# Kernel tuning notes

Hardware: AMD Instinct MI355X
Metric: run time of the kernel (lower is better)

The kernel has to match this reference:

```python
import jax, jax.numpy as jnp
import numpy as np

B, N, DIM, H, DH, EDGE_DIM = 2, 320, 512, 8, 64, 64
INNER = H * DH  # 512


def setup_inputs() -> dict:
    key = jax.random.key(0)
    ks = jax.random.split(key, 8)
    s = jnp.float32(0.02)
    f32 = jnp.float32
    return {
        "nodes": jax.random.normal(ks[0], (B, N, DIM), f32),
        "edges": jax.random.normal(ks[1], (B, EDGE_DIM, N, N), f32),
        "W_exp": jax.random.normal(ks[2], (DIM, INNER), f32) * s,
        "b_exp": jnp.zeros((INNER,), f32),
        "W_q": jax.random.normal(ks[3], (INNER, INNER), f32) * s,
        "b_q": jnp.zeros((INNER,), f32),
        "W_kv": jax.random.normal(ks[4], (INNER, 2 * INNER), f32) * s,
        "b_kv": jnp.zeros((2 * INNER,), f32),
        "W_e": jax.random.normal(ks[5], (EDGE_DIM, INNER), f32) * s,
        "b_e": jnp.zeros((INNER,), f32),
        "W_out": jax.random.normal(ks[6], (INNER, DIM), f32) * s,
        "b_out": jnp.zeros((DIM,), f32),
    }


def reference(nodes, edges, W_exp, b_exp, W_q, b_q, W_kv, b_kv, W_e, b_e, W_out, b_out):
    b, n, _ = nodes.shape
    h, dh = H, DH
    scale = dh ** -0.5

    x = nodes @ W_exp + b_exp                      # [b, n, inner]
    q = x @ W_q + b_q                              # [b, n, inner]
    kv = x @ W_kv + b_kv
    k, v = jnp.split(kv, 2, axis=-1)               # each [b, n, inner]

    def split_heads(t):
        return t.reshape(b, n, h, dh).transpose(0, 2, 1, 3)  # [b, h, n, dh]

    q, k, v = map(split_heads, (q, k, v))

    # edges: [b, edge_dim, i, j] -> projected edge k/v bias [b, h, i, j, dh]
    e = jnp.einsum('beij,ed->bijd', edges, W_e) + b_e
    e = e.reshape(b, n, n, h, dh).transpose(0, 3, 1, 2, 4)

    # sim = q . (k + e); split into matmul term + edge term (same math)
    sim = (jnp.einsum('bhid,bhjd->bhij', q, k)
           + jnp.einsum('bhid,bhijd->bhij', q, e)) * scale
    attn = jax.nn.softmax(sim, axis=-1)            # [b, h, i, j]

    # out = attn . (v + e)
    out = (jnp.einsum('bhij,bhjd->bhid', attn, v)
           + jnp.einsum('bhij,bhijd->bhid', attn, e))
    out = out.transpose(0, 2, 1, 3).reshape(b, n, h * dh)  # [b, n, inner]
    return out @ W_out + b_out
```

## Files before the change

kernel.cpp:

```cpp
#include <hip/hip_runtime.h>

#define B_  2
#define N_  320
#define H_  8
#define ED_ 64

typedef __attribute__((ext_vector_type(8))) short bf16x8;
typedef __attribute__((ext_vector_type(4))) float floatx4;

__device__ __forceinline__ ushort f2bf(float f) {
    union { float f; unsigned u; } c; c.f = f;
    unsigned u = c.u;
    return (ushort)((u + 0x7fffu + ((u >> 16) & 1u)) >> 16);
}
__device__ __forceinline__ float bf2f(ushort s) {
    union { unsigned u; float f; } c; c.u = ((unsigned)s) << 16;
    return c.f;
}
__device__ __forceinline__ uint4 packf8(const float* f) {
    uint4 r;
    r.x = (unsigned)f2bf(f[0]) | ((unsigned)f2bf(f[1]) << 16);
    r.y = (unsigned)f2bf(f[2]) | ((unsigned)f2bf(f[3]) << 16);
    r.z = (unsigned)f2bf(f[4]) | ((unsigned)f2bf(f[5]) << 16);
    r.w = (unsigned)f2bf(f[6]) | ((unsigned)f2bf(f[7]) << 16);
    return r;
}
__device__ __forceinline__ uint4 packu8(const ushort* s) {
    uint4 r;
    r.x = (unsigned)s[0] | ((unsigned)s[1] << 16);
    r.y = (unsigned)s[2] | ((unsigned)s[3] << 16);
    r.z = (unsigned)s[4] | ((unsigned)s[5] << 16);
    r.w = (unsigned)s[6] | ((unsigned)s[7] << 16);
    return r;
}

__global__ __launch_bounds__(256) void prep_kernel(
    const float* __restrict__ W_exp, const float* __restrict__ W_q,
    const float* __restrict__ W_kv, const float* __restrict__ W_out,
    const float* __restrict__ W_e,
    ushort* __restrict__ WT_exp, ushort* __restrict__ WT_qkv,
    ushort* __restrict__ WT_oh, ushort* __restrict__ WT_ol,
    float* __restrict__ W_eT, ushort* __restrict__ Wehi, ushort* __restrict__ Welo)
{
    __shared__ float T[64][65];
    const int id = blockIdx.x, tid = threadIdx.x;

    if (id >= 320) {
        const int c0 = (id - 320) * 64;
        const int r = tid >> 2, cs = (tid & 3) * 16;
        #pragma unroll
        for (int e = 0; e < 4; ++e) {
            float4 x4 = *(const float4*)&W_e[(long)r * 512 + c0 + cs + e * 4];
            T[r][cs + e*4] = x4.x; T[r][cs + e*4 + 1] = x4.y;
            T[r][cs + e*4 + 2] = x4.z; T[r][cs + e*4 + 3] = x4.w;
        }
        __syncthreads();
        const int cc = tid >> 2, ks = (tid & 3) * 16;
        const int hd = c0 + cc;
        float vals[16]; ushort hs[16], ls[16];
        #pragma unroll
        for (int e = 0; e < 16; ++e) {
            vals[e] = T[ks + e][cc];
            hs[e] = f2bf(vals[e]);
            ls[e] = f2bf(vals[e] - bf2f(hs[e]));
        }
        #pragma unroll
        for (int e = 0; e < 4; ++e) {
            float4 o4; o4.x = vals[e*4]; o4.y = vals[e*4+1]; o4.z = vals[e*4+2]; o4.w = vals[e*4+3];
            *(float4*)&W_eT[(long)hd * 64 + ks + e * 4] = o4;
        }
        *(uint4*)&Wehi[(long)hd * 64 + ks]     = packu8(hs);
        *(uint4*)&Wehi[(long)hd * 64 + ks + 8] = packu8(hs + 8);
        *(uint4*)&Welo[(long)hd * 64 + ks]     = packu8(ls);
        *(uint4*)&Welo[(long)hd * 64 + ks + 8] = packu8(ls + 8);
        return;
    }
    const float* src; ushort* dst; ushort* dstl = nullptr;
    int ldS, row0, kt, ct;
    if (id < 64)       { int l = id;       kt = l >> 3; ct = l & 7;  src = W_exp; ldS = 512;  dst = WT_exp; row0 = ct * 64; }
    else if (id < 128) { int l = id - 64;  kt = l >> 3; ct = l & 7;  src = W_q;   ldS = 512;  dst = WT_qkv; row0 = ct * 64; }
    else if (id < 256) { int l = id - 128; kt = l >> 4; ct = l & 15; src = W_kv;  ldS = 1024; dst = WT_qkv; row0 = 512 + ct * 64; }
    else               { int l = id - 256; kt = l >> 3; ct = l & 7;  src = W_out; ldS = 512;  dst = WT_oh; dstl = WT_ol; row0 = ct * 64; }
    const int k0 = kt * 64, c0 = ct * 64;
    {
        const int r = tid >> 2, cs = (tid & 3) * 16;
        #pragma unroll
        for (int e = 0; e < 4; ++e) {
            float4 x4 = *(const float4*)&src[(long)(k0 + r) * ldS + c0 + cs + e * 4];
            T[r][cs + e*4] = x4.x; T[r][cs + e*4 + 1] = x4.y;
            T[r][cs + e*4 + 2] = x4.z; T[r][cs + e*4 + 3] = x4.w;
        }
    }
    __syncthreads();
    {
        const int cc = tid >> 2, ks = (tid & 3) * 16;
        float vals[16];
        #pragma unroll
        for (int e = 0; e < 16; ++e) vals[e] = T[ks + e][cc];
        ushort* d = dst + (long)(row0 + cc) * 512 + k0 + ks;
        if (!dstl) {
            *(uint4*)d = packf8(vals);
            *(uint4*)(d + 8) = packf8(vals + 8);
        } else {
            ushort hs[16], ls[16];
            #pragma unroll
            for (int e = 0; e < 16; ++e) {
                hs[e] = f2bf(vals[e]);
                ls[e] = f2bf(vals[e] - bf2f(hs[e]));
            }
            *(uint4*)d = packu8(hs);
            *(uint4*)(d + 8) = packu8(hs + 8);
            ushort* d2 = dstl + (long)(row0 + cc) * 512 + k0 + ks;
            *(uint4*)d2 = packu8(ls);
            *(uint4*)(d2 + 8) = packu8(ls + 8);
        }
    }
}

template <int MODE>
__global__ __launch_bounds__(256) void gemm_v2(
    const void* __restrict__ Asrc, const ushort* __restrict__ WT,
    const float* __restrict__ bias1, const float* __restrict__ bias2,
    ushort* __restrict__ outbf, float* __restrict__ q_o,
    float* __restrict__ k_o, float* __restrict__ vt_o)
{
    __shared__ ushort As[64 * 64];
    __shared__ ushort Bs[64 * 64];
    __shared__ float  T[64][65];
    const int tid = threadIdx.x, lane = tid & 63, wid = tid >> 6;
    const int wr = wid >> 1, wc = wid & 1;
    const int bm = blockIdx.x * 64, bn = blockIdx.y * 64;
    const int srow = tid >> 2, sk = tid & 3;
    const int sw = (srow & 7) << 4;
    const int d1 = srow * 128 + ((sk * 32) ^ sw);
    const int d2 = srow * 128 + ((sk * 32 + 16) ^ sw);
    const ushort* Bsrc = WT + (long)(bn + srow) * 512 + sk * 16;

    floatx4 acc[2][2] = {};
    for (int k0 = 0; k0 < 512; k0 += 64) {
        uint4 a0, a1;
        if (MODE == 0) {
            const float* ap = (const float*)Asrc + (long)(bm + srow) * 512 + k0 + sk * 16;
            float f[16];
            #pragma unroll
            for (int e = 0; e < 4; ++e) {
                float4 x4 = *(const float4*)(ap + e * 4);
                f[e*4] = x4.x; f[e*4+1] = x4.y; f[e*4+2] = x4.z; f[e*4+3] = x4.w;
            }
            a0 = packf8(f); a1 = packf8(f + 8);
        } else {
            const ushort* ap = (const ushort*)Asrc + (long)(bm + srow) * 512 + k0 + sk * 16;
            a0 = *(const uint4*)ap; a1 = *(const uint4*)(ap + 8);
        }
        uint4 b0 = *(const uint4*)(Bsrc + k0);
        uint4 b1 = *(const uint4*)(Bsrc + k0 + 8);
        if (k0) __syncthreads();
        *(uint4*)((char*)As + d1) = a0;
        *(uint4*)((char*)As + d2) = a1;
        *(uint4*)((char*)Bs + d1) = b0;
        *(uint4*)((char*)Bs + d2) = b1;
        __syncthreads();
        #pragma unroll
        for (int s = 0; s < 2; ++s) {
            const int kb = s * 64 + ((lane >> 4) * 16);
            bf16x8 af[2], bfr[2];
            #pragma unroll
            for (int mf = 0; mf < 2; ++mf) {
                int row = wr * 32 + mf * 16 + (lane & 15);
                af[mf] = *(const bf16x8*)((const char*)As + row * 128 + (kb ^ ((row & 7) << 4)));
            }
            #pragma unroll
            for (int nf = 0; nf < 2; ++nf) {
                int col = wc * 32 + nf * 16 + (lane & 15);
                bfr[nf] = *(const bf16x8*)((const char*)Bs + col * 128 + (kb ^ ((col & 7) << 4)));
            }
            #pragma unroll
            for (int mf = 0; mf < 2; ++mf)
                #pragma unroll
                for (int nf = 0; nf < 2; ++nf)
                    acc[mf][nf] = __builtin_amdgcn_mfma_f32_16x16x32_bf16(
                        af[mf], bfr[nf], acc[mf][nf], 0, 0, 0);
        }
    }
    const int r4 = (lane >> 4) * 4, c16 = lane & 15;
    if (MODE == 0) {
        #pragma unroll
        for (int mf = 0; mf < 2; ++mf)
            #pragma unroll
            for (int nf = 0; nf < 2; ++nf)
                #pragma unroll
                for (int j = 0; j < 4; ++j) {
                    int row = bm + wr * 32 + mf * 16 + r4 + j;
                    int cn  = bn + wc * 32 + nf * 16 + c16;
                    outbf[(long)row * 512 + cn] = f2bf(acc[mf][nf][j] + bias1[cn]);
                }
    } else {
        const int cat = blockIdx.y >> 3;
        if (cat == 0) {
            #pragma unroll
            for (int mf = 0; mf < 2; ++mf)
                #pragma unroll
                for (int nf = 0; nf < 2; ++nf)
                    #pragma unroll
                    for (int j = 0; j < 4; ++j) {
                        int row = bm + wr * 32 + mf * 16 + r4 + j;
                        int cn  = bn + wc * 32 + nf * 16 + c16;
                        q_o[(long)row * 512 + cn] = acc[mf][nf][j] + bias1[cn];
                    }
        } else if (cat == 1) {
            #pragma unroll
            for (int mf = 0; mf < 2; ++mf)
                #pragma unroll
                for (int nf = 0; nf < 2; ++nf)
                    #pragma unroll
                    for (int j = 0; j < 4; ++j) {
                        int row = bm + wr * 32 + mf * 16 + r4 + j;
                        int cn  = bn + wc * 32 + nf * 16 + c16;
                        k_o[(long)row * 512 + (cn - 512)] = acc[mf][nf][j] + bias2[cn - 512];
                    }
        } else {
            #pragma unroll
            for (int mf = 0; mf < 2; ++mf)
                #pragma unroll
                for (int nf = 0; nf < 2; ++nf)
                    #pragma unroll
                    for (int j = 0; j < 4; ++j) {
                        int rl = wr * 32 + mf * 16 + r4 + j;
                        int cl = wc * 32 + nf * 16 + c16;
                        T[rl][cl] = acc[mf][nf][j] + bias2[bn - 512 + cl];
                    }
            __syncthreads();
            const int cl = tid >> 2, rl4 = (tid & 3) * 16;
            const int bb = bm / N_, ii0 = bm % N_, cv0 = bn - 1024;
            const long orow = (long)bb * 512 + cv0 + cl;
            #pragma unroll
            for (int e4 = 0; e4 < 4; ++e4) {
                float4 o4;
                o4.x = T[rl4 + e4*4 + 0][cl]; o4.y = T[rl4 + e4*4 + 1][cl];
                o4.z = T[rl4 + e4*4 + 2][cl]; o4.w = T[rl4 + e4*4 + 3][cl];
                *(float4*)&vt_o[orow * N_ + ii0 + rl4 + e4*4] = o4;
            }
        }
    }
}

__global__ __launch_bounds__(256) void k_qk(
    const float* __restrict__ q, const float* __restrict__ k,
    float* __restrict__ S_g)
{
    __shared__ ushort Qh[64 * 64], Ql[64 * 64], Kt[320 * 64];
    const int it = blockIdx.x, bh = blockIdx.y;
    const int b = bh >> 3, h = bh & 7;
    const int tid = threadIdx.x, lane = tid & 63, wid = tid >> 6;
    const int srow = tid >> 2, sk = tid & 3;
    const int sw = (srow & 7) << 4;
    const int d1 = srow * 128 + ((sk * 32) ^ sw);
    const int d2 = srow * 128 + ((sk * 32 + 16) ^ sw);

    {
        const float* ap = q + (long)(b * N_ + it * 64 + srow) * 512 + h * 64 + sk * 16;
        float f[16]; ushort hs[16], ls[16];
        #pragma unroll
        for (int e = 0; e < 4; ++e) {
            float4 x4 = *(const float4*)(ap + e * 4);
            f[e*4] = 0.125f * x4.x; f[e*4+1] = 0.125f * x4.y;
            f[e*4+2] = 0.125f * x4.z; f[e*4+3] = 0.125f * x4.w;
        }
        #pragma unroll
        for (int e = 0; e < 16; ++e) {
            hs[e] = f2bf(f[e]);
            ls[e] = f2bf(f[e] - bf2f(hs[e]));
        }
        *(uint4*)((char*)Qh + d1) = packu8(hs);
        *(uint4*)((char*)Qh + d2) = packu8(hs + 8);
        *(uint4*)((char*)Ql + d1) = packu8(ls);
        *(uint4*)((char*)Ql + d2) = packu8(ls + 8);
    }
    #pragma unroll
    for (int p = 0; p < 5; ++p) {
        const int row = p * 64 + srow;
        const float* kp = k + (long)(b * N_ + row) * 512 + h * 64 + sk * 16;
        float f[16];
        #pragma unroll
        for (int e = 0; e < 4; ++e) {
            float4 x4 = *(const float4*)(kp + e * 4);
            f[e*4] = x4.x; f[e*4+1] = x4.y; f[e*4+2] = x4.z; f[e*4+3] = x4.w;
        }
        *(uint4*)((char*)Kt + row * 128 + ((sk * 32) ^ sw))      = packf8(f);
        *(uint4*)((char*)Kt + row * 128 + ((sk * 32 + 16) ^ sw)) = packf8(f + 8);
    }
    __syncthreads();

    const int j0w = wid * 80;
    floatx4 acc[4][5] = {};
    #pragma unroll
    for (int s = 0; s < 2; ++s) {
        const int kb = s * 64 + ((lane >> 4) * 16);
        bf16x8 afh[4], afl[4], bf[5];
        #pragma unroll
        for (int mf = 0; mf < 4; ++mf) {
            int row = mf * 16 + (lane & 15);
            int off = row * 128 + (kb ^ ((row & 7) << 4));
            afh[mf] = *(const bf16x8*)((const char*)Qh + off);
            afl[mf] = *(const bf16x8*)((const char*)Ql + off);
        }
        #pragma unroll
        for (int jt = 0; jt < 5; ++jt) {
            int row = j0w + jt * 16 + (lane & 15);
            bf[jt] = *(const bf16x8*)((const char*)Kt + row * 128 + (kb ^ ((row & 7) << 4)));
        }
        #pragma unroll
        for (int mf = 0; mf < 4; ++mf)
            #pragma unroll
            for (int jt = 0; jt < 5; ++jt) {
                acc[mf][jt] = __builtin_amdgcn_mfma_f32_16x16x32_bf16(afh[mf], bf[jt], acc[mf][jt], 0, 0, 0);
                acc[mf][jt] = __builtin_amdgcn_mfma_f32_16x16x32_bf16(afl[mf], bf[jt], acc[mf][jt], 0, 0, 0);
            }
    }
    const int r4 = (lane >> 4) * 4, c16 = lane & 15;
    #pragma unroll
    for (int mf = 0; mf < 4; ++mf)
        #pragma unroll
        for (int jt = 0; jt < 5; ++jt)
            #pragma unroll
            for (int e = 0; e < 4; ++e) {
                int ri = it * 64 + mf * 16 + r4 + e;
                int cj = j0w + jt * 16 + c16;
                S_g[((long)bh * N_ + ri) * N_ + cj] = acc[mf][jt][e];
            }
}

__global__ __launch_bounds__(512) void attn_kernel(
    const float* __restrict__ q, const float* __restrict__ S_g,
    const float* __restrict__ edges, const float* __restrict__ W_eT,
    ushort* __restrict__ A_g, float* __restrict__ U_g)
{
    __shared__ ushort E_s[64 * 324];
    __shared__ ushort A_lds[8 * 320];
    __shared__ float  q_lds[512];
    __shared__ float  t_lds[512];

    const int blk = blockIdx.x;
    const int b = blk / N_, i = blk % N_;
    const int tid = threadIdx.x;
    const int w = tid >> 6, lane = tid & 63;

    q_lds[tid] = q[(long)blk * 512 + tid];
    {
        const float* ebase = edges + (long)b * ED_ * N_ * N_ + (long)i * N_;
        for (int idx = tid; idx < 64 * 80; idx += 512) {
            int c = idx / 80, j4 = (idx % 80) * 4;
            float4 e4 = *(const float4*)(ebase + (long)c * (N_ * N_) + j4);
            uint2 pk;
            pk.x = (unsigned)f2bf(e4.x) | ((unsigned)f2bf(e4.y) << 16);
            pk.y = (unsigned)f2bf(e4.z) | ((unsigned)f2bf(e4.w) << 16);
            *(uint2*)&E_s[c * 324 + j4] = pk;
        }
    }
    __syncthreads();

    {
        float tacc = 0.f;
        const float* we = W_eT + (long)(w * 64) * 64 + lane;
        const float* ql = q_lds + w * 64;
        #pragma unroll 8
        for (int d = 0; d < 64; ++d) tacc += ql[d] * we[(long)d * 64];
        t_lds[tid] = tacc;
    }
    __syncthreads();

    float sacc[5] = {0.f, 0.f, 0.f, 0.f, 0.f};
    {
        const float* tl = t_lds + w * 64;
        #pragma unroll 4
        for (int c = 0; c < 64; ++c) {
            float tc = tl[c];
            const ushort* er = &E_s[c * 324 + lane];
            sacc[0] += tc * bf2f(er[0]);
            sacc[1] += tc * bf2f(er[64]);
            sacc[2] += tc * bf2f(er[128]);
            sacc[3] += tc * bf2f(er[192]);
            sacc[4] += tc * bf2f(er[256]);
        }
    }
    const long sbase = ((long)(b * 8 + w) * N_ + i) * N_ + lane;
    const float scale = 0.125f;
    float s0 = sacc[0] * scale + S_g[sbase];
    float s1 = sacc[1] * scale + S_g[sbase + 64];
    float s2 = sacc[2] * scale + S_g[sbase + 128];
    float s3 = sacc[3] * scale + S_g[sbase + 192];
    float s4 = sacc[4] * scale + S_g[sbase + 256];

    float m = fmaxf(fmaxf(fmaxf(s0, s1), fmaxf(s2, s3)), s4);
    #pragma unroll
    for (int off = 32; off >= 1; off >>= 1) m = fmaxf(m, __shfl_xor(m, off, 64));
    s0 = __expf(s0 - m); s1 = __expf(s1 - m); s2 = __expf(s2 - m);
    s3 = __expf(s3 - m); s4 = __expf(s4 - m);
    float sum = s0 + s1 + s2 + s3 + s4;
    #pragma unroll
    for (int off = 32; off >= 1; off >>= 1) sum += __shfl_xor(sum, off, 64);
    float inv = 1.f / sum;
    ushort a0 = f2bf(s0 * inv), a1 = f2bf(s1 * inv), a2 = f2bf(s2 * inv),
           a3 = f2bf(s3 * inv), a4 = f2bf(s4 * inv);
    A_lds[w * 320 + lane]       = a0;
    A_lds[w * 320 + 64 + lane]  = a1;
    A_lds[w * 320 + 128 + lane] = a2;
    A_lds[w * 320 + 192 + lane] = a3;
    A_lds[w * 320 + 256 + lane] = a4;
    A_g[sbase]       = a0;
    A_g[sbase + 64]  = a1;
    A_g[sbase + 128] = a2;
    A_g[sbase + 192] = a3;
    A_g[sbase + 256] = a4;
    __syncthreads();

    float acc_u = 0.f;
    {
        const ushort* Er = E_s + lane * 324;
        const ushort* Ar = A_lds + w * 320;
        #pragma unroll 4
        for (int j4 = 0; j4 < 80; ++j4) {
            uint2 aa = *(const uint2*)&Ar[j4 * 4];
            uint2 e2 = *(const uint2*)&Er[j4 * 4];
            acc_u += bf2f((ushort)(aa.x & 0xffffu)) * bf2f((ushort)(e2.x & 0xffffu));
            acc_u += bf2f((ushort)(aa.x >> 16))     * bf2f((ushort)(e2.x >> 16));
            acc_u += bf2f((ushort)(aa.y & 0xffffu)) * bf2f((ushort)(e2.y & 0xffffu));
            acc_u += bf2f((ushort)(aa.y >> 16))     * bf2f((ushort)(e2.y >> 16));
        }
    }
    U_g[((long)(b * 8 + w) * N_ + i) * 64 + lane] = acc_u;
}

__global__ __launch_bounds__(256) void k_ov(
    const ushort* __restrict__ A_g, const float* __restrict__ vt,
    const float* __restrict__ U_g, const ushort* __restrict__ Wh_g,
    const ushort* __restrict__ Wl_g, const float* __restrict__ b_e,
    float* __restrict__ o_out)
{
    __shared__ ushort B0[64 * 64], B1[64 * 64], B2[64 * 64], B3[64 * 64];
    const int it = blockIdx.x, bh = blockIdx.y;
    const int b = bh >> 3, h = bh & 7;
    const int tid = threadIdx.x, lane = tid & 63, wid = tid >> 6;
    const int wr = wid >> 1, wc = wid & 1;
    const int srow = tid >> 2, sk = tid & 3;
    const int sw = (srow & 7) << 4;
    const int d1 = srow * 128 + ((sk * 32) ^ sw);
    const int d2 = srow * 128 + ((sk * 32 + 16) ^ sw);

    floatx4 acc[2][2] = {};
    for (int j0 = 0; j0 < 320; j0 += 64) {
        const ushort* ap = A_g + ((long)bh * N_ + it * 64 + srow) * N_ + j0 + sk * 16;
        uint4 a0 = *(const uint4*)ap, a1 = *(const uint4*)(ap + 8);
        const float* vp = vt + ((long)b * 512 + h * 64 + srow) * N_ + j0 + sk * 16;
        float f[16]; ushort hs[16], ls[16];
        #pragma unroll
        for (int e = 0; e < 4; ++e) {
            float4 x4 = *(const float4*)(vp + e * 4);
            f[e*4] = x4.x; f[e*4+1] = x4.y; f[e*4+2] = x4.z; f[e*4+3] = x4.w;
        }
        #pragma unroll
        for (int e = 0; e < 16; ++e) {
            hs[e] = f2bf(f[e]);
            ls[e] = f2bf(f[e] - bf2f(hs[e]));
        }
        if (j0) __syncthreads();
        *(uint4*)((char*)B0 + d1) = a0;
        *(uint4*)((char*)B0 + d2) = a1;
        *(uint4*)((char*)B1 + d1) = packu8(hs);
        *(uint4*)((char*)B1 + d2) = packu8(hs + 8);
        *(uint4*)((char*)B2 + d1) = packu8(ls);
        *(uint4*)((char*)B2 + d2) = packu8(ls + 8);
        __syncthreads();
        #pragma unroll
        for (int s = 0; s < 2; ++s) {
            const int kb = s * 64 + ((lane >> 4) * 16);
            bf16x8 af[2], bh_[2], bl_[2];
            #pragma unroll
            for (int mf = 0; mf < 2; ++mf) {
                int row = wr * 32 + mf * 16 + (lane & 15);
                af[mf] = *(const bf16x8*)((const char*)B0 + row * 128 + (kb ^ ((row & 7) << 4)));
            }
            #pragma unroll
            for (int nf = 0; nf < 2; ++nf) {
                int col = wc * 32 + nf * 16 + (lane & 15);
                int off = col * 128 + (kb ^ ((col & 7) << 4));
                bh_[nf] = *(const bf16x8*)((const char*)B1 + off);
                bl_[nf] = *(const bf16x8*)((const char*)B2 + off);
            }
            #pragma unroll
            for (int mf = 0; mf < 2; ++mf)
                #pragma unroll
                for (int nf = 0; nf < 2; ++nf) {
                    acc[mf][nf] = __builtin_amdgcn_mfma_f32_16x16x32_bf16(af[mf], bh_[nf], acc[mf][nf], 0, 0, 0);
                    acc[mf][nf] = __builtin_amdgcn_mfma_f32_16x16x32_bf16(af[mf], bl_[nf], acc[mf][nf], 0, 0, 0);
                }
        }
    }
    {
        const float* up = U_g + ((long)bh * N_ + it * 64 + srow) * 64 + sk * 16;
        float f[16]; ushort uh[16], ul[16];
        #pragma unroll
        for (int e = 0; e < 4; ++e) {
            float4 x4 = *(const float4*)(up + e * 4);
            f[e*4] = x4.x; f[e*4+1] = x4.y; f[e*4+2] = x4.z; f[e*4+3] = x4.w;
        }
        #pragma unroll
        for (int e = 0; e < 16; ++e) {
            uh[e] = f2bf(f[e]);
            ul[e] = f2bf(f[e] - bf2f(uh[e]));
        }
        const ushort* whp = Wh_g + ((long)h * 64 + srow) * 64 + sk * 16;
        const ushort* wlp = Wl_g + ((long)h * 64 + srow) * 64 + sk * 16;
        uint4 w0 = *(const uint4*)whp, w1 = *(const uint4*)(whp + 8);
        uint4 x0 = *(const uint4*)wlp, x1 = *(const uint4*)(wlp + 8);
        __syncthreads();
        *(uint4*)((char*)B0 + d1) = packu8(uh);
        *(uint4*)((char*)B0 + d2) = packu8(uh + 8);
        *(uint4*)((char*)B1 + d1) = packu8(ul);
        *(uint4*)((char*)B1 + d2) = packu8(ul + 8);
        *(uint4*)((char*)B2 + d1) = w0;
        *(uint4*)((char*)B2 + d2) = w1;
        *(uint4*)((char*)B3 + d1) = x0;
        *(uint4*)((char*)B3 + d2) = x1;
        __syncthreads();
        #pragma unroll
        for (int s = 0; s < 2; ++s) {
            const int kb = s * 64 + ((lane >> 4) * 16);
            bf16x8 ah[2], al[2], wh_[2], wl_[2];
            #pragma unroll
            for (int mf = 0; mf < 2; ++mf) {
                int row = wr * 32 + mf * 16 + (lane & 15);
                int off = row * 128 + (kb ^ ((row & 7) << 4));
                ah[mf] = *(const bf16x8*)((const char*)B0 + off);
                al[mf] = *(const bf16x8*)((const char*)B1 + off);
            }
            #pragma unroll
            for (int nf = 0; nf < 2; ++nf) {
                int col = wc * 32 + nf * 16 + (lane & 15);
                int off = col * 128 + (kb ^ ((col & 7) << 4));
                wh_[nf] = *(const bf16x8*)((const char*)B2 + off);
                wl_[nf] = *(const bf16x8*)((const char*)B3 + off);
            }
            #pragma unroll
            for (int mf = 0; mf < 2; ++mf)
                #pragma unroll
                for (int nf = 0; nf < 2; ++nf) {
                    acc[mf][nf] = __builtin_amdgcn_mfma_f32_16x16x32_bf16(ah[mf], wh_[nf], acc[mf][nf], 0, 0, 0);
                    acc[mf][nf] = __builtin_amdgcn_mfma_f32_16x16x32_bf16(al[mf], wh_[nf], acc[mf][nf], 0, 0, 0);
                    acc[mf][nf] = __builtin_amdgcn_mfma_f32_16x16x32_bf16(ah[mf], wl_[nf], acc[mf][nf], 0, 0, 0);
                }
        }
    }
    const int r4 = (lane >> 4) * 4, c16 = lane & 15;
    #pragma unroll
    for (int mf = 0; mf < 2; ++mf)
        #pragma unroll
        for (int nf = 0; nf < 2; ++nf)
            #pragma unroll
            for (int e = 0; e < 4; ++e) {
                int row = it * 64 + wr * 32 + mf * 16 + r4 + e;
                int col = wc * 32 + nf * 16 + c16;
                o_out[((long)(b * N_ + row)) * 512 + h * 64 + col] =
                    acc[mf][nf][e] + b_e[h * 64 + col];
            }
}

__global__ __launch_bounds__(256) void gemm_out(
    const float* __restrict__ Af, const ushort* __restrict__ BTh,
    const ushort* __restrict__ BTl, const float* __restrict__ bias,
    float* __restrict__ C)
{
    __shared__ ushort Ah[64 * 64], Al[64 * 64], Bh[64 * 64], Bl[64 * 64];
    const int tid = threadIdx.x, lane = tid & 63, wid = tid >> 6;
    const int wr = wid >> 1, wc = wid & 1;
    const int bm = blockIdx.x * 64, bn = blockIdx.y * 64;
    const int srow = tid >> 2, sk = tid & 3;
    const int sw = (srow & 7) << 4;
    const int d1 = srow * 128 + ((sk * 32) ^ sw);
    const int d2 = srow * 128 + ((sk * 32 + 16) ^ sw);
    const float*  asrc = Af + (long)(bm + srow) * 512 + sk * 16;
    const ushort* bhs  = BTh + (long)(bn + srow) * 512 + sk * 16;
    const ushort* bls  = BTl + (long)(bn + srow) * 512 + sk * 16;

    floatx4 acc[2][2] = {};
    for (int k0 = 0; k0 < 512; k0 += 64) {
        float f[16];
        #pragma unroll
        for (int e = 0; e < 4; ++e) {
            float4 x4 = *(const float4*)(asrc + k0 + e * 4);
            f[e*4] = x4.x; f[e*4+1] = x4.y; f[e*4+2] = x4.z; f[e*4+3] = x4.w;
        }
        ushort hs[16], ls[16];
        #pragma unroll
        for (int e = 0; e < 16; ++e) {
            hs[e] = f2bf(f[e]);
            ls[e] = f2bf(f[e] - bf2f(hs[e]));
        }
        uint4 bh0 = *(const uint4*)(bhs + k0);
        uint4 bh1 = *(const uint4*)(bhs + k0 + 8);
        uint4 bl0 = *(const uint4*)(bls + k0);
        uint4 bl1 = *(const uint4*)(bls + k0 + 8);
        if (k0) __syncthreads();
        *(uint4*)((char*)Ah + d1) = packu8(hs);
        *(uint4*)((char*)Ah + d2) = packu8(hs + 8);
        *(uint4*)((char*)Al + d1) = packu8(ls);
        *(uint4*)((char*)Al + d2) = packu8(ls + 8);
        *(uint4*)((char*)Bh + d1) = bh0;
        *(uint4*)((char*)Bh + d2) = bh1;
        *(uint4*)((char*)Bl + d1) = bl0;
        *(uint4*)((char*)Bl + d2) = bl1;
        __syncthreads();
        #pragma unroll
        for (int s = 0; s < 2; ++s) {
            const int kb = s * 64 + ((lane >> 4) * 16);
            bf16x8 ah[2], al[2], bh[2], bl[2];
            #pragma unroll
            for (int mf = 0; mf < 2; ++mf) {
                int row = wr * 32 + mf * 16 + (lane & 15);
                int off = row * 128 + (kb ^ ((row & 7) << 4));
                ah[mf] = *(const bf16x8*)((const char*)Ah + off);
                al[mf] = *(const bf16x8*)((const char*)Al + off);
            }
            #pragma unroll
            for (int nf = 0; nf < 2; ++nf) {
                int col = wc * 32 + nf * 16 + (lane & 15);
                int off = col * 128 + (kb ^ ((col & 7) << 4));
                bh[nf] = *(const bf16x8*)((const char*)Bh + off);
                bl[nf] = *(const bf16x8*)((const char*)Bl + off);
            }
            #pragma unroll
            for (int mf = 0; mf < 2; ++mf)
                #pragma unroll
                for (int nf = 0; nf < 2; ++nf) {
                    acc[mf][nf] = __builtin_amdgcn_mfma_f32_16x16x32_bf16(ah[mf], bh[nf], acc[mf][nf], 0, 0, 0);
                    acc[mf][nf] = __builtin_amdgcn_mfma_f32_16x16x32_bf16(ah[mf], bl[nf], acc[mf][nf], 0, 0, 0);
                    acc[mf][nf] = __builtin_amdgcn_mfma_f32_16x16x32_bf16(al[mf], bh[nf], acc[mf][nf], 0, 0, 0);
                }
        }
    }
    const int r4 = (lane >> 4) * 4, c16 = lane & 15;
    #pragma unroll
    for (int mf = 0; mf < 2; ++mf)
        #pragma unroll
        for (int nf = 0; nf < 2; ++nf)
            #pragma unroll
            for (int j = 0; j < 4; ++j) {
                int row = bm + wr * 32 + mf * 16 + r4 + j;
                int col = bn + wc * 32 + nf * 16 + c16;
                C[(long)row * 512 + col] = acc[mf][nf][j] + bias[col];
            }
}

extern "C" void kernel_launch(void* const* d_in, const int* in_sizes, int n_in,
                              void* d_out, int out_size, void* d_ws, size_t ws_size,
                              hipStream_t stream)
{
    const float* nodes = (const float*)d_in[0];
    const float* edges = (const float*)d_in[1];
    const float* W_exp = (const float*)d_in[2];
    const float* b_exp = (const float*)d_in[3];
    const float* W_q   = (const float*)d_in[4];
    const float* b_q   = (const float*)d_in[5];
    const float* W_kv  = (const float*)d_in[6];
    const float* b_kv  = (const float*)d_in[7];
    const float* W_e   = (const float*)d_in[8];
    const float* b_e   = (const float*)d_in[9];
    const float* W_out = (const float*)d_in[10];
    const float* b_out = (const float*)d_in[11];
    float* out = (float*)d_out;

    const long SZ = (long)B_ * N_ * 512;
    float* ws   = (float*)d_ws;
    float* q    = ws;
    float* k    = ws + SZ;
    float* v_t  = ws + 2 * SZ;
    float* U_g  = ws + 3 * SZ;
    float* S    = ws + 3 * SZ + 131072;
    float* o    = S;
    ushort* A_g    = (ushort*)(S + 1638400);
    ushort* x_bf   = A_g + 1638400;
    ushort* WT_exp = x_bf + SZ;
    ushort* WT_qkv = WT_exp + 262144;
    ushort* WT_oh  = WT_qkv + 786432;
    ushort* WT_ol  = WT_oh + 262144;
    float*  W_eT   = (float*)(WT_ol + 262144);
    ushort* Wehi   = (ushort*)(W_eT + 32768);
    ushort* Welo   = Wehi + 32768;

    prep_kernel<<<328, 256, 0, stream>>>(W_exp, W_q, W_kv, W_out, W_e,
                                         WT_exp, WT_qkv, WT_oh, WT_ol,
                                         W_eT, Wehi, Welo);
    gemm_v2<0><<<dim3(10, 8), 256, 0, stream>>>(nodes, WT_exp, b_exp, nullptr,
                                                x_bf, nullptr, nullptr, nullptr);
    gemm_v2<1><<<dim3(10, 24), 256, 0, stream>>>(x_bf, WT_qkv, b_q, b_kv,
                                                 nullptr, q, k, v_t);
    k_qk<<<dim3(5, 16), 256, 0, stream>>>(q, k, S);
    attn_kernel<<<640, 512, 0, stream>>>(q, S, edges, W_eT, A_g, U_g);
    k_ov<<<dim3(5, 16), 256, 0, stream>>>(A_g, v_t, U_g, Wehi, Welo, b_e, o);
    gemm_out<<<dim3(10, 8), 256, 0, stream>>>(o, WT_oh, WT_ol, b_out, out);
}
```

Before: 177.2 us.

## Store q/k/v as head-major bf16 and use MFMA for edge-score and edge-value terms

The QKV GEMM epilogue now writes q (pre-scaled by 1/sqrt(dh)), k and v directly as bf16 in head-major layout. This removes the fp32 round trips and the hi/lo split-bf16 conversions in k_qk and k_ov, which also halves their MFMA count. In attn_kernel, the edge-score dot product (t·E) and the A·E edge-value reduction move from scalar FMA loops to bf16 MFMA tiles, with partial scores staged in LDS. The cost is lower precision, since q, v and t now go through a single bf16 instead of the hi+lo pair, and attn_kernel uses more LDS.

New measurement: 162.6 us. -8.2%, faster.

```diff
diff --git a/kernel.cpp b/kernel.cpp
--- a/kernel.cpp
+++ b/kernel.cpp
@@ -32,6 +32,9 @@
     r.z = (unsigned)s[4] | ((unsigned)s[5] << 16);
     r.w = (unsigned)s[6] | ((unsigned)s[7] << 16);
     return r;
+}
+__device__ __forceinline__ bf16x8 u4bf(uint4 u) {
+    union { uint4 u; bf16x8 b; } c; c.u = u; return c.b;
 }
 
 __global__ __launch_bounds__(256) void prep_kernel(
@@ -121,8 +124,8 @@
 __global__ __launch_bounds__(256) void gemm_v2(
     const void* __restrict__ Asrc, const ushort* __restrict__ WT,
     const float* __restrict__ bias1, const float* __restrict__ bias2,
-    ushort* __restrict__ outbf, float* __restrict__ q_o,
-    float* __restrict__ k_o, float* __restrict__ vt_o)
+    ushort* __restrict__ outbf, ushort* __restrict__ q_bf,
+    ushort* __restrict__ k_bf, ushort* __restrict__ v_bf)
 {
     __shared__ ushort As[64 * 64];
     __shared__ ushort Bs[64 * 64];
@@ -197,6 +200,7 @@
     } else {
         const int cat = blockIdx.y >> 3;
         if (cat == 0) {
+            const int h = blockIdx.y;
             #pragma unroll
             for (int mf = 0; mf < 2; ++mf)
                 #pragma unroll
@@ -204,10 +208,13 @@
                     #pragma unroll
                     for (int j = 0; j < 4; ++j) {
                         int row = bm + wr * 32 + mf * 16 + r4 + j;
-                        int cn  = bn + wc * 32 + nf * 16 + c16;
-                        q_o[(long)row * 512 + cn] = acc[mf][nf][j] + bias1[cn];
+                        int bb = row / N_, ii = row - bb * N_;
+                        int d = wc * 32 + nf * 16 + c16;
+                        q_bf[(((long)bb * 8 + h) * N_ + ii) * 64 + d] =
+                            f2bf(0.125f * (acc[mf][nf][j] + bias1[h * 64 + d]));
                     }
         } else if (cat == 1) {
+            const int h = blockIdx.y - 8;
             #pragma unroll
             for (int mf = 0; mf < 2; ++mf)
                 #pragma unroll
@@ -215,8 +222,10 @@
                     #pragma unroll
                     for (int j = 0; j < 4; ++j) {
                         int row = bm + wr * 32 + mf * 16 + r4 + j;
-                        int cn  = bn + wc * 32 + nf * 16 + c16;
-                        k_o[(long)row * 512 + (cn - 512)] = acc[mf][nf][j] + bias2[cn - 512];
+                        int bb = row / N_, ii = row - bb * N_;
+                        int d = wc * 32 + nf * 16 + c16;
+                        k_bf[(((long)bb * 8 + h) * N_ + ii) * 64 + d] =
+                            f2bf(acc[mf][nf][j] + bias2[h * 64 + d]);
                     }
         } else {
             #pragma unroll
@@ -233,61 +242,38 @@
             const int cl = tid >> 2, rl4 = (tid & 3) * 16;
             const int bb = bm / N_, ii0 = bm % N_, cv0 = bn - 1024;
             const long orow = (long)bb * 512 + cv0 + cl;
-            #pragma unroll
-            for (int e4 = 0; e4 < 4; ++e4) {
-                float4 o4;
-                o4.x = T[rl4 + e4*4 + 0][cl]; o4.y = T[rl4 + e4*4 + 1][cl];
-                o4.z = T[rl4 + e4*4 + 2][cl]; o4.w = T[rl4 + e4*4 + 3][cl];
-                *(float4*)&vt_o[orow * N_ + ii0 + rl4 + e4*4] = o4;
-            }
+            ushort tmp[16];
+            #pragma unroll
+            for (int e = 0; e < 16; ++e) tmp[e] = f2bf(T[rl4 + e][cl]);
+            *(uint4*)&v_bf[orow * N_ + ii0 + rl4]     = packu8(tmp);
+            *(uint4*)&v_bf[orow * N_ + ii0 + rl4 + 8] = packu8(tmp + 8);
         }
     }
 }
 
 __global__ __launch_bounds__(256) void k_qk(
-    const float* __restrict__ q, const float* __restrict__ k,
+    const ushort* __restrict__ qbf, const ushort* __restrict__ kbf,
     float* __restrict__ S_g)
 {
-    __shared__ ushort Qh[64 * 64], Ql[64 * 64], Kt[320 * 64];
+    __shared__ ushort Qs[64 * 64], Ks[320 * 64];
     const int it = blockIdx.x, bh = blockIdx.y;
-    const int b = bh >> 3, h = bh & 7;
     const int tid = threadIdx.x, lane = tid & 63, wid = tid >> 6;
     const int srow = tid >> 2, sk = tid & 3;
     const int sw = (srow & 7) << 4;
-    const int d1 = srow * 128 + ((sk * 32) ^ sw);
-    const int d2 = srow * 128 + ((sk * 32 + 16) ^ sw);
+    const int d1b = ((sk * 32) ^ sw);
+    const int d2b = ((sk * 32 + 16) ^ sw);
 
     {
-        const float* ap = q + (long)(b * N_ + it * 64 + srow) * 512 + h * 64 + sk * 16;
-        float f[16]; ushort hs[16], ls[16];
-        #pragma unroll
-        for (int e = 0; e < 4; ++e) {
-            float4 x4 = *(const float4*)(ap + e * 4);
-            f[e*4] = 0.125f * x4.x; f[e*4+1] = 0.125f * x4.y;
-            f[e*4+2] = 0.125f * x4.z; f[e*4+3] = 0.125f * x4.w;
-        }
-        #pragma unroll
-        for (int e = 0; e < 16; ++e) {
-            hs[e] = f2bf(f[e]);
-            ls[e] = f2bf(f[e] - bf2f(hs[e]));
-        }
-        *(uint4*)((char*)Qh + d1) = packu8(hs);
-        *(uint4*)((char*)Qh + d2) = packu8(hs + 8);
-        *(uint4*)((char*)Ql + d1) = packu8(ls);
-        *(uint4*)((char*)Ql + d2) = packu8(ls + 8);
+        const ushort* qp = qbf + ((long)bh * N_ + it * 64 + srow) * 64 + sk * 16;
+        *(uint4*)((char*)Qs + srow * 128 + d1b) = *(const uint4*)qp;
+        *(uint4*)((char*)Qs + srow * 128 + d2b) = *(const uint4*)(qp + 8);
     }
     #pragma unroll
     for (int p = 0; p < 5; ++p) {
         const int row = p * 64 + srow;
-        const float* kp = k + (long)(b * N_ + row) * 512 + h * 64 + sk * 16;
-        float f[16];
-        #pragma unroll
-        for (int e = 0; e < 4; ++e) {
-            float4 x4 = *(const float4*)(kp + e * 4);
-            f[e*4] = x4.x; f[e*4+1] = x4.y; f[e*4+2] = x4.z; f[e*4+3] = x4.w;
-        }
-        *(uint4*)((char*)Kt + row * 128 + ((sk * 32) ^ sw))      = packf8(f);
-        *(uint4*)((char*)Kt + row * 128 + ((sk * 32 + 16) ^ sw)) = packf8(f + 8);
+        const ushort* kp = kbf + ((long)bh * N_ + row) * 64 + sk * 16;
+        *(uint4*)((char*)Ks + row * 128 + d1b) = *(const uint4*)kp;
+        *(uint4*)((char*)Ks + row * 128 + d2b) = *(const uint4*)(kp + 8);
     }
     __syncthreads();
 
@@ -296,26 +282,22 @@
     #pragma unroll
     for (int s = 0; s < 2; ++s) {
         const int kb = s * 64 + ((lane >> 4) * 16);
-        bf16x8 afh[4], afl[4], bf[5];
+        bf16x8 af[4], bf[5];
         #pragma unroll
         for (int mf = 0; mf < 4; ++mf) {
             int row = mf * 16 + (lane & 15);
-            int off = row * 128 + (kb ^ ((row & 7) << 4));
-            afh[mf] = *(const bf16x8*)((const char*)Qh + off);
-            afl[mf] = *(const bf16x8*)((const char*)Ql + off);
+            af[mf] = *(const bf16x8*)((const char*)Qs + row * 128 + (kb ^ ((row & 7) << 4)));
         }
         #pragma unroll
         for (int jt = 0; jt < 5; ++jt) {
             int row = j0w + jt * 16 + (lane & 15);
-            bf[jt] = *(const bf16x8*)((const char*)Kt + row * 128 + (kb ^ ((row & 7) << 4)));
+            bf[jt] = *(const bf16x8*)((const char*)Ks + row * 128 + (kb ^ ((row & 7) << 4)));
         }
         #pragma unroll
         for (int mf = 0; mf < 4; ++mf)
             #pragma unroll
-            for (int jt = 0; jt < 5; ++jt) {
-                acc[mf][jt] = __builtin_amdgcn_mfma_f32_16x16x32_bf16(afh[mf], bf[jt], acc[mf][jt], 0, 0, 0);
-                acc[mf][jt] = __builtin_amdgcn_mfma_f32_16x16x32_bf16(afl[mf], bf[jt], acc[mf][jt], 0, 0, 0);
-            }
+            for (int jt = 0; jt < 5; ++jt)
+                acc[mf][jt] = __builtin_amdgcn_mfma_f32_16x16x32_bf16(af[mf], bf[jt], acc[mf][jt], 0, 0, 0);
     }
     const int r4 = (lane >> 4) * 4, c16 = lane & 15;
     #pragma unroll
@@ -331,21 +313,21 @@
 }
 
 __global__ __launch_bounds__(512) void attn_kernel(
-    const float* __restrict__ q, const float* __restrict__ S_g,
+    const ushort* __restrict__ qbf, const float* __restrict__ S_g,
     const float* __restrict__ edges, const float* __restrict__ W_eT,
     ushort* __restrict__ A_g, float* __restrict__ U_g)
 {
     __shared__ ushort E_s[64 * 324];
+    __shared__ float  t_lds[1024];
+    __shared__ float  S_lds[8 * 320];
     __shared__ ushort A_lds[8 * 320];
-    __shared__ float  q_lds[512];
-    __shared__ float  t_lds[512];
 
     const int blk = blockIdx.x;
     const int b = blk / N_, i = blk % N_;
     const int tid = threadIdx.x;
     const int w = tid >> 6, lane = tid & 63;
-
-    q_lds[tid] = q[(long)blk * 512 + tid];
+    const int r16 = lane & 15, kq = (lane >> 4) * 8;
+
     {
         const float* ebase = edges + (long)b * ED_ * N_ * N_ + (long)i * N_;
         for (int idx = tid; idx < 64 * 80; idx += 512) {
@@ -357,40 +339,57 @@
             *(uint2*)&E_s[c * 324 + j4] = pk;
         }
     }
-    __syncthreads();
-
     {
         float tacc = 0.f;
-        const float* we = W_eT + (long)(w * 64) * 64 + lane;
-        const float* ql = q_lds + w * 64;
+        const ushort* qp = qbf + ((long)(b * 8 + w) * N_ + i) * 64;
+        const float* wp = W_eT + (long)(w * 64) * 64 + lane;
         #pragma unroll 8
-        for (int d = 0; d < 64; ++d) tacc += ql[d] * we[(long)d * 64];
+        for (int d = 0; d < 64; ++d) tacc += bf2f(qp[d]) * wp[(long)d * 64];
         t_lds[tid] = tacc;
+        t_lds[512 + tid] = 0.f;
     }
     __syncthreads();
 
-    float sacc[5] = {0.f, 0.f, 0.f, 0.f, 0.f};
     {
-        const float* tl = t_lds + w * 64;
-        #pragma unroll 4
-        for (int c = 0; c < 64; ++c) {
-            float tc = tl[c];
-            const ushort* er = &E_s[c * 324 + lane];
-            sacc[0] += tc * bf2f(er[0]);
-            sacc[1] += tc * bf2f(er[64]);
-            sacc[2] += tc * bf2f(er[128]);
-            sacc[3] += tc * bf2f(er[192]);
-            sacc[4] += tc * bf2f(er[256]);
-        }
-    }
+        bf16x8 ta[2];
+        #pragma unroll
+        for (int s = 0; s < 2; ++s) {
+            const float* tp = &t_lds[r16 * 64 + s * 32 + kq];
+            bf16x8 v;
+            #pragma unroll
+            for (int e = 0; e < 8; ++e) v[e] = (short)f2bf(tp[e]);
+            ta[s] = v;
+        }
+        int tl[3]; int nt = 2;
+        tl[0] = w * 2; tl[1] = w * 2 + 1; tl[2] = 0;
+        if (w < 4) { tl[2] = 16 + w; nt = 3; }
+        for (int ti = 0; ti < nt; ++ti) {
+            const int j0 = tl[ti] * 16;
+            floatx4 acc = {0.f, 0.f, 0.f, 0.f};
+            #pragma unroll
+            for (int s = 0; s < 2; ++s) {
+                bf16x8 eb;
+                #pragma unroll
+                for (int e = 0; e < 8; ++e)
+                    eb[e] = (short)E_s[(s * 32 + kq + e) * 324 + j0 + r16];
+                acc = __builtin_amdgcn_mfma_f32_16x16x32_bf16(ta[s], eb, acc, 0, 0, 0);
+            }
+            if (lane < 32) {
+                const int rr = (lane >> 4) * 4;
+                #pragma unroll
+                for (int jj = 0; jj < 4; ++jj)
+                    S_lds[(rr + jj) * 320 + j0 + r16] = acc[jj];
+            }
+        }
+    }
+    __syncthreads();
+
     const long sbase = ((long)(b * 8 + w) * N_ + i) * N_ + lane;
-    const float scale = 0.125f;
-    float s0 = sacc[0] * scale + S_g[sbase];
-    float s1 = sacc[1] * scale + S_g[sbase + 64];
-    float s2 = sacc[2] * scale + S_g[sbase + 128];
-    float s3 = sacc[3] * scale + S_g[sbase + 192];
-    float s4 = sacc[4] * scale + S_g[sbase + 256];
-
+    float s0 = S_lds[w * 320 + lane]       + S_g[sbase];
+    float s1 = S_lds[w * 320 + 64 + lane]  + S_g[sbase + 64];
+    float s2 = S_lds[w * 320 + 128 + lane] + S_g[sbase + 128];
+    float s3 = S_lds[w * 320 + 192 + lane] + S_g[sbase + 192];
+    float s4 = S_lds[w * 320 + 256 + lane] + S_g[sbase + 256];
     float m = fmaxf(fmaxf(fmaxf(s0, s1), fmaxf(s2, s3)), s4);
     #pragma unroll
     for (int off = 32; off >= 1; off >>= 1) m = fmaxf(m, __shfl_xor(m, off, 64));
@@ -414,25 +413,33 @@
     A_g[sbase + 256] = a4;
     __syncthreads();
 
-    float acc_u = 0.f;
-    {
-        const ushort* Er = E_s + lane * 324;
-        const ushort* Ar = A_lds + w * 320;
-        #pragma unroll 4
-        for (int j4 = 0; j4 < 80; ++j4) {
-            uint2 aa = *(const uint2*)&Ar[j4 * 4];
-            uint2 e2 = *(const uint2*)&Er[j4 * 4];
-            acc_u += bf2f((ushort)(aa.x & 0xffffu)) * bf2f((ushort)(e2.x & 0xffffu));
-            acc_u += bf2f((ushort)(aa.x >> 16))     * bf2f((ushort)(e2.x >> 16));
-            acc_u += bf2f((ushort)(aa.y & 0xffffu)) * bf2f((ushort)(e2.y & 0xffffu));
-            acc_u += bf2f((ushort)(aa.y >> 16))     * bf2f((ushort)(e2.y >> 16));
-        }
-    }
-    U_g[((long)(b * 8 + w) * N_ + i) * 64 + lane] = acc_u;
+    if (w < 4) {
+        const int c0 = w * 16;
+        const bool rl = r16 < 8;
+        const int arow = r16 & 7;
+        floatx4 acc = {0.f, 0.f, 0.f, 0.f};
+        #pragma unroll 2
+        for (int ks = 0; ks < 10; ++ks) {
+            const int jb = ks * 32 + kq;
+            uint4 av = *(const uint4*)&A_lds[arow * 320 + jb];
+            if (!rl) { av.x = 0; av.y = 0; av.z = 0; av.w = 0; }
+            const ushort* ep = &E_s[(c0 + r16) * 324 + jb];
+            uint2 e0 = *(const uint2*)ep;
+            uint2 e1 = *(const uint2*)(ep + 4);
+            uint4 bv; bv.x = e0.x; bv.y = e0.y; bv.z = e1.x; bv.w = e1.y;
+            acc = __builtin_amdgcn_mfma_f32_16x16x32_bf16(u4bf(av), u4bf(bv), acc, 0, 0, 0);
+        }
+        if (lane < 32) {
+            const int rr = (lane >> 4) * 4;
+            #pragma unroll
+            for (int jj = 0; jj < 4; ++jj)
+                U_g[((long)(b * 8 + rr + jj) * N_ + i) * 64 + c0 + r16] = acc[jj];
+        }
+    }
 }
 
 __global__ __launch_bounds__(256) void k_ov(
-    const ushort* __restrict__ A_g, const float* __restrict__ vt,
+    const ushort* __restrict__ A_g, const ushort* __restrict__ v_bf,
     const float* __restrict__ U_g, const ushort* __restrict__ Wh_g,
     const ushort* __restrict__ Wl_g, const float* __restrict__ b_e,
     float* __restrict__ o_out)
@@ -451,30 +458,18 @@
     for (int j0 = 0; j0 < 320; j0 += 64) {
         const ushort* ap = A_g + ((long)bh * N_ + it * 64 + srow) * N_ + j0 + sk * 16;
         uint4 a0 = *(const uint4*)ap, a1 = *(const uint4*)(ap + 8);
-        const float* vp = vt + ((long)b * 512 + h * 64 + srow) * N_ + j0 + sk * 16;
-        float f[16]; ushort hs[16], ls[16];
-        #pragma unroll
-        for (int e = 0; e < 4; ++e) {
-            float4 x4 = *(const float4*)(vp + e * 4);
-            f[e*4] = x4.x; f[e*4+1] = x4.y; f[e*4+2] = x4.z; f[e*4+3] = x4.w;
-        }
-        #pragma unroll
-        for (int e = 0; e < 16; ++e) {
-            hs[e] = f2bf(f[e]);
-            ls[e] = f2bf(f[e] - bf2f(hs[e]));
-        }
+        const ushort* vp = v_bf + ((long)b * 512 + h * 64 + srow) * N_ + j0 + sk * 16;
+        uint4 v0 = *(const uint4*)vp, v1 = *(const uint4*)(vp + 8);
         if (j0) __syncthreads();
         *(uint4*)((char*)B0 + d1) = a0;
         *(uint4*)((char*)B0 + d2) = a1;
-        *(uint4*)((char*)B1 + d1) = packu8(hs);
-        *(uint4*)((char*)B1 + d2) = packu8(hs + 8);
-        *(uint4*)((char*)B2 + d1) = packu8(ls);
-        *(uint4*)((char*)B2 + d2) = packu8(ls + 8);
+        *(uint4*)((char*)B1 + d1) = v0;
+        *(uint4*)((char*)B1 + d2) = v1;
         __syncthreads();
         #pragma unroll
         for (int s = 0; s < 2; ++s) {
             const int kb = s * 64 + ((lane >> 4) * 16);
-            bf16x8 af[2], bh_[2], bl_[2];
+            bf16x8 af[2], vh_[2];
             #pragma unroll
             for (int mf = 0; mf < 2; ++mf) {
                 int row = wr * 32 + mf * 16 + (lane & 15);
@@ -483,17 +478,13 @@
             #pragma unroll
             for (int nf = 0; nf < 2; ++nf) {
                 int col = wc * 32 + nf * 16 + (lane & 15);
-                int off = col * 128 + (kb ^ ((col & 7) << 4));
-                bh_[nf] = *(const bf16x8*)((const char*)B1 + off);
-                bl_[nf] = *(const bf16x8*)((const char*)B2 + off);
+                vh_[nf] = *(const bf16x8*)((const char*)B1 + col * 128 + (kb ^ ((col & 7) << 4)));
             }
             #pragma unroll
             for (int mf = 0; mf < 2; ++mf)
                 #pragma unroll
-                for (int nf = 0; nf < 2; ++nf) {
-                    acc[mf][nf] = __builtin_amdgcn_mfma_f32_16x16x32_bf16(af[mf], bh_[nf], acc[mf][nf], 0, 0, 0);
-                    acc[mf][nf] = __builtin_amdgcn_mfma_f32_16x16x32_bf16(af[mf], bl_[nf], acc[mf][nf], 0, 0, 0);
-                }
+                for (int nf = 0; nf < 2; ++nf)
+                    acc[mf][nf] = __builtin_amdgcn_mfma_f32_16x16x32_bf16(af[mf], vh_[nf], acc[mf][nf], 0, 0, 0);
         }
     }
     {
@@ -670,21 +661,21 @@
     float* out = (float*)d_out;
 
     const long SZ = (long)B_ * N_ * 512;
-    float* ws   = (float*)d_ws;
-    float* q    = ws;
-    float* k    = ws + SZ;
-    float* v_t  = ws + 2 * SZ;
-    float* U_g  = ws + 3 * SZ;
-    float* S    = ws + 3 * SZ + 131072;
-    float* o    = S;
-    ushort* A_g    = (ushort*)(S + 1638400);
+    float* ws = (float*)d_ws;
+    float*  S_g  = ws;
+    float*  o    = ws;
+    float*  U_g  = ws + 1638400;
+    float*  W_eT = ws + 1966080;
+    ushort* A_g    = (ushort*)(ws + 1998848);
     ushort* x_bf   = A_g + 1638400;
-    ushort* WT_exp = x_bf + SZ;
+    ushort* q_bf   = x_bf + 327680;
+    ushort* k_bf   = q_bf + 327680;
+    ushort* v_bf   = k_bf + 327680;
+    ushort* WT_exp = v_bf + 327680;
     ushort* WT_qkv = WT_exp + 262144;
     ushort* WT_oh  = WT_qkv + 786432;
     ushort* WT_ol  = WT_oh + 262144;
-    float*  W_eT   = (float*)(WT_ol + 262144);
-    ushort* Wehi   = (ushort*)(W_eT + 32768);
+    ushort* Wehi   = WT_ol + 262144;
     ushort* Welo   = Wehi + 32768;
 
     prep_kernel<<<328, 256, 0, stream>>>(W_exp, W_q, W_kv, W_out, W_e,
@@ -693,9 +684,9 @@
     gemm_v2<0><<<dim3(10, 8), 256, 0, stream>>>(nodes, WT_exp, b_exp, nullptr,
                                                 x_bf, nullptr, nullptr, nullptr);
     gemm_v2<1><<<dim3(10, 24), 256, 0, stream>>>(x_bf, WT_qkv, b_q, b_kv,
-                                                 nullptr, q, k, v_t);
-    k_qk<<<dim3(5, 16), 256, 0, stream>>>(q, k, S);
-    attn_kernel<<<640, 512, 0, stream>>>(q, S, edges, W_eT, A_g, U_g);
-    k_ov<<<dim3(5, 16), 256, 0, stream>>>(A_g, v_t, U_g, Wehi, Welo, b_e, o);
+                                                 nullptr, q_bf, k_bf, v_bf);
+    k_qk<<<dim3(5, 16), 256, 0, stream>>>(q_bf, k_bf, S_g);
+    attn_kernel<<<640, 512, 0, stream>>>(q_bf, S_g, edges, W_eT, A_g, U_g);
+    k_ov<<<dim3(5, 16), 256, 0, stream>>>(A_g, v_bf, U_g, Wehi, Welo, b_e, o);
     gemm_out<<<dim3(10, 8), 256, 0, stream>>>(o, WT_oh, WT_ol, b_out, out);
 }
```
